# Performance work log

Measured on AMD Instinct MI355X. Metric: run time of the kernel, lower is better.

## Reference

```python
import jax, jax.numpy as jnp
from jax import lax
import numpy as np

B, T, F, H = 64, 512, 256, 512


def _gru_scan(data_tbf, Wi, bi, Wh, bhn):
    """Run a flax-style GRUCell over time. data_tbf: (T, B, F) -> (T, B, H)."""
    def step(h, x):
        xg = x @ Wi + bi              # (B, 3H): ir | iz | in
        hg = h @ Wh                   # (B, 3H): hr | hz | hn (hn bias added below)
        xr, xz, xn = jnp.split(xg, 3, axis=-1)
        hr, hz, hn = jnp.split(hg, 3, axis=-1)
        r = jax.nn.sigmoid(xr + hr)
        z = jax.nn.sigmoid(xz + hz)
        n = jnp.tanh(xn + r * (hn + bhn))
        new_h = (1.0 - z) * n + z * h
        return new_h, new_h

    h0 = jnp.zeros((data_tbf.shape[1], Wh.shape[0]), data_tbf.dtype)
    _, ys = lax.scan(step, h0, data_tbf)
    return ys


def setup_inputs() -> dict:
    key = jax.random.key(0)
    ks = jax.random.split(key, 5)
    s_i = 1.0 / np.sqrt(F)
    s_h = 1.0 / np.sqrt(H)
    return {
        "data": jax.random.normal(ks[0], (B, T, F), jnp.float32),
        "Wi_f": jax.random.normal(ks[1], (F, 3 * H), jnp.float32) * s_i,
        "bi_f": jnp.zeros((3 * H,), jnp.float32),
        "Wh_f": jax.random.normal(ks[2], (H, 3 * H), jnp.float32) * s_h,
        "bhn_f": jnp.zeros((H,), jnp.float32),
        "Wi_b": jax.random.normal(ks[3], (F, 3 * H), jnp.float32) * s_i,
        "bi_b": jnp.zeros((3 * H,), jnp.float32),
        "Wh_b": jax.random.normal(ks[4], (H, 3 * H), jnp.float32) * s_h,
        "bhn_b": jnp.zeros((H,), jnp.float32),
    }


def reference(data, Wi_f, bi_f, Wh_f, bhn_f, Wi_b, bi_b, Wh_b, bhn_b):
    # Forward direction: scan over time (axis 1 of data)
    fwd = _gru_scan(jnp.swapaxes(data, 0, 1), Wi_f, bi_f, Wh_f, bhn_f)
    fwd = jnp.swapaxes(fwd, 0, 1)                      # (B, T, H)
    # 'Backward' direction: source flips axis 0 (batch), faithfully reproduced.
    rev = jnp.flip(data, axis=0)
    bwd = _gru_scan(jnp.swapaxes(rev, 0, 1), Wi_b, bi_b, Wh_b, bhn_b)
    bwd = jnp.swapaxes(bwd, 0, 1)                      # (B, T, H)
    bwd = jnp.flip(bwd, axis=0)
    return jnp.concatenate([fwd, bwd], axis=-1)        # (B, T, 2H)
```

## Files before the change

### kernel.cpp

```cpp
#include <hip/hip_runtime.h>
#include <hip/hip_bf16.h>


#define TT 512
#define FF 256
#define HH 512
#define G3 1536
#define NSLICE 32
#define NWG 256
#define NTHR 64

typedef __attribute__((ext_vector_type(8))) short short8;
typedef __attribute__((ext_vector_type(4))) float f32x4;

__device__ __forceinline__ unsigned short f2bf(float f) {
  union { float f; unsigned u; } x; x.f = f;
  return (unsigned short)((x.u + 0x7fffu + ((x.u >> 16) & 1u)) >> 16);
}

__device__ __forceinline__ unsigned pk2(float a, float b) {
  union { __hip_bfloat162 h; unsigned u; } x;
  x.h = __float22bfloat162_rn(make_float2(a, b));
  return x.u;
}

__device__ __forceinline__ float sigm(float x) {
  return __builtin_amdgcn_rcpf(1.f + __expf(-x));
}

#define MFMA(a, b, c) __builtin_amdgcn_mfma_f32_16x16x32_bf16((a), (b), (c), 0, 0, 0)

__global__ __launch_bounds__(NTHR, 1) void gru_fused(
    const float* __restrict__ data,
    const float* __restrict__ Wi_f, const float* __restrict__ bi_f,
    const float* __restrict__ Wh_f, const float* __restrict__ bhn_f,
    const float* __restrict__ Wi_b, const float* __restrict__ bi_b,
    const float* __restrict__ Wh_b, const float* __restrict__ bhn_b,
    float* __restrict__ out,
    unsigned long long* __restrict__ hbuf,
    int* __restrict__ flags)
{
  const int wg   = blockIdx.x;
  const int unit = wg & 7;
  const int s    = wg >> 3;
  const int dir  = unit >> 2;
  const int bg   = unit & 3;
  const int lane = threadIdx.x;
  const int l15  = lane & 15;
  const int lg   = lane >> 4;

  const float* Wi  = dir ? Wi_b  : Wi_f;
  const float* Wh  = dir ? Wh_b  : Wh_f;
  const float* bi  = dir ? bi_b  : bi_f;
  const float* bhn = dir ? bhn_b : bhn_f;

  const int colT = s * 16 + l15;
  const int colBase = s * 16 + lg * 4;

  short8 whf[3][16];
#pragma unroll
  for (int g = 0; g < 3; ++g)
#pragma unroll
    for (int ks = 0; ks < 16; ++ks) {
      short8 v;
#pragma unroll
      for (int j = 0; j < 8; ++j)
        v[j] = (short)f2bf(Wh[(size_t)(ks * 32 + lg * 8 + j) * G3 + g * HH + colT]);
      whf[g][ks] = v;
    }
  short8 wif[3][8];
#pragma unroll
  for (int g = 0; g < 3; ++g)
#pragma unroll
    for (int ks = 0; ks < 8; ++ks) {
      short8 v;
#pragma unroll
      for (int j = 0; j < 8; ++j)
        v[j] = (short)f2bf(Wi[(size_t)(ks * 32 + lg * 8 + j) * G3 + g * HH + colT]);
      wif[g][ks] = v;
    }
  float biR[4], biZ[4], biN[4], bhc[4];
#pragma unroll
  for (int j = 0; j < 4; ++j) {
    biR[j] = bi[colBase + j];
    biZ[j] = bi[HH + colBase + j];
    biN[j] = bi[2 * HH + colBase + j];
    bhc[j] = bhn[colBase + j];
  }

  int* myflags = flags + unit * 32;
  const float* xbase = data + (size_t)(bg * 16 + l15) * TT * FF;

  float hp[4] = {0.f, 0.f, 0.f, 0.f};

  for (int t = 0; t < TT; ++t) {
    const int ib = t & 1;

    f32x4 accR = {0.f, 0.f, 0.f, 0.f};
    f32x4 accZ = {0.f, 0.f, 0.f, 0.f};
    f32x4 xN   = {0.f, 0.f, 0.f, 0.f};
    {
      const float* xr = xbase + (size_t)t * FF;
#pragma unroll
      for (int ks = 0; ks < 8; ++ks) {
        float4 x0 = *(const float4*)(xr + ks * 32 + lg * 8);
        float4 x1 = *(const float4*)(xr + ks * 32 + lg * 8 + 4);
        union { short8 s; unsigned u[4]; } a;
        a.u[0] = pk2(x0.x, x0.y); a.u[1] = pk2(x0.z, x0.w);
        a.u[2] = pk2(x1.x, x1.y); a.u[3] = pk2(x1.z, x1.w);
        accR = MFMA(wif[0][ks], a.s, accR);
        accZ = MFMA(wif[1][ks], a.s, accZ);
        xN   = MFMA(wif[2][ks], a.s, xN);
      }
    }

    if (t > 0) {
      const int fidx = lane & 31;
      while (true) {
        int fl = __hip_atomic_load(&myflags[fidx], __ATOMIC_RELAXED, __HIP_MEMORY_SCOPE_AGENT);
        if (__all(fl >= t)) break;
      }
      asm volatile("" ::: "memory");
    }

    const unsigned long long* hin = hbuf + (size_t)(unit * 2 + ib) * 2048;
    unsigned long long q[32];
#pragma unroll
    for (int ks = 0; ks < 16; ++ks) {
      const int bidx = l15 * 128 + ks * 8 + lg * 2;
      q[2 * ks]     = __hip_atomic_load(&hin[bidx],     __ATOMIC_RELAXED, __HIP_MEMORY_SCOPE_AGENT);
      q[2 * ks + 1] = __hip_atomic_load(&hin[bidx + 1], __ATOMIC_RELAXED, __HIP_MEMORY_SCOPE_AGENT);
    }

    f32x4 hN = {0.f, 0.f, 0.f, 0.f};
#pragma unroll
    for (int ks = 0; ks < 16; ++ks) {
      union { short8 s; unsigned long long q[2]; } a;
      a.q[0] = q[2 * ks]; a.q[1] = q[2 * ks + 1];
      accR = MFMA(whf[0][ks], a.s, accR);
      accZ = MFMA(whf[1][ks], a.s, accZ);
      hN   = MFMA(whf[2][ks], a.s, hN);
    }

    float hv[4];
#pragma unroll
    for (int j = 0; j < 4; ++j) {
      float r = sigm(accR[j] + biR[j]);
      float z = sigm(accZ[j] + biZ[j]);
      float e = __expf(2.f * (xN[j] + biN[j] + r * (hN[j] + bhc[j])));
      float n = 1.f - 2.f * __builtin_amdgcn_rcpf(e + 1.f);
      hv[j] = (1.f - z) * n + z * hp[j];
      hp[j] = hv[j];
    }

    unsigned long long pv = (unsigned long long)pk2(hv[0], hv[1])
                          | ((unsigned long long)pk2(hv[2], hv[3]) << 32);
    unsigned long long* hout = hbuf + (size_t)(unit * 2 + (ib ^ 1)) * 2048;
    __hip_atomic_store(&hout[l15 * 128 + s * 4 + lg], pv,
                       __ATOMIC_RELAXED, __HIP_MEMORY_SCOPE_AGENT);
    asm volatile("s_waitcnt vmcnt(0)" ::: "memory");
    if (lane == 0)
      __hip_atomic_store(&myflags[s], t + 1, __ATOMIC_RELAXED, __HIP_MEMORY_SCOPE_AGENT);

    *(float4*)(out + ((size_t)(bg * 16 + l15) * TT + t) * 1024 + (size_t)dir * HH + colBase)
        = make_float4(hv[0], hv[1], hv[2], hv[3]);
  }
}

extern "C" void kernel_launch(void* const* d_in, const int* in_sizes, int n_in,
                              void* d_out, int out_size, void* d_ws, size_t ws_size,
                              hipStream_t stream) {
  const float* data  = (const float*)d_in[0];
  const float* Wi_f  = (const float*)d_in[1];
  const float* bi_f  = (const float*)d_in[2];
  const float* Wh_f  = (const float*)d_in[3];
  const float* bhn_f = (const float*)d_in[4];
  const float* Wi_b  = (const float*)d_in[5];
  const float* bi_b  = (const float*)d_in[6];
  const float* Wh_b  = (const float*)d_in[7];
  const float* bhn_b = (const float*)d_in[8];
  float* out = (float*)d_out;

  unsigned long long* hbuf = (unsigned long long*)d_ws;
  int* flags = (int*)((char*)d_ws + 262144);
  hipMemsetAsync(d_ws, 0, 262144 + 4096, stream);

  gru_fused<<<NWG, NTHR, 0, stream>>>(data, Wi_f, bi_f, Wh_f, bhn_f,
                                      Wi_b, bi_b, Wh_b, bhn_b, out, hbuf, flags);
}
```

Before: 3.732 ms.

## Replace flag-based step barrier with per-element tagged hidden-state exchange

Drops the separate per-slice flag array and the store-wait-then-flag handshake. Each bf16 hidden value is now packed with a 16-bit timestep tag in a 32-bit word, and readers poll the hidden buffer itself with cache-bypassing loads until every tag matches. This takes a full memory round trip (vmcnt wait plus flag publish) off the serial critical path of each timestep. In exchange the exchange buffer doubles in size, the polling loads reread the whole hidden vector on each retry, and correctness relies on each 64-bit half being stored atomically with its tags.

```diff
diff --git a/kernel.cpp b/kernel.cpp
--- a/kernel.cpp
+++ b/kernel.cpp
@@ -6,12 +6,15 @@
 #define FF 256
 #define HH 512
 #define G3 1536
-#define NSLICE 32
 #define NWG 256
 #define NTHR 64
 
 typedef __attribute__((ext_vector_type(8))) short short8;
 typedef __attribute__((ext_vector_type(4))) float f32x4;
+typedef unsigned int u32;
+typedef unsigned long long u64;
+
+union U4 { uint4 v; u32 u[4]; u64 q[2]; };
 
 __device__ __forceinline__ unsigned short f2bf(float f) {
   union { float f; unsigned u; } x; x.f = f;
@@ -37,8 +40,7 @@
     const float* __restrict__ Wi_b, const float* __restrict__ bi_b,
     const float* __restrict__ Wh_b, const float* __restrict__ bhn_b,
     float* __restrict__ out,
-    unsigned long long* __restrict__ hbuf,
-    int* __restrict__ flags)
+    u32* __restrict__ hbuf)
 {
   const int wg   = blockIdx.x;
   const int unit = wg & 7;
@@ -88,14 +90,10 @@
     bhc[j] = bhn[colBase + j];
   }
 
-  int* myflags = flags + unit * 32;
   const float* xbase = data + (size_t)(bg * 16 + l15) * TT * FF;
-
   float hp[4] = {0.f, 0.f, 0.f, 0.f};
 
   for (int t = 0; t < TT; ++t) {
-    const int ib = t & 1;
-
     f32x4 accR = {0.f, 0.f, 0.f, 0.f};
     f32x4 accZ = {0.f, 0.f, 0.f, 0.f};
     f32x4 xN   = {0.f, 0.f, 0.f, 0.f};
@@ -114,29 +112,38 @@
       }
     }
 
-    if (t > 0) {
-      const int fidx = lane & 31;
-      while (true) {
-        int fl = __hip_atomic_load(&myflags[fidx], __ATOMIC_RELAXED, __HIP_MEMORY_SCOPE_AGENT);
-        if (__all(fl >= t)) break;
+    const u32 tag = (u32)t;
+    const u32* hb = hbuf + ((size_t)(unit * 2 + (t & 1)) << 13);
+    U4 q[32];
+    while (true) {
+#pragma unroll
+      for (int ks = 0; ks < 16; ++ks) {
+        const u32* p = hb + l15 * 512 + ks * 32 + lg * 8;
+        asm volatile("global_load_dwordx4 %0, %1, off sc0 sc1"
+                     : "=v"(q[2 * ks].v) : "v"(p));
+        asm volatile("global_load_dwordx4 %0, %1, off sc0 sc1"
+                     : "=v"(q[2 * ks + 1].v) : "v"(p + 4));
       }
-      asm volatile("" ::: "memory");
-    }
-
-    const unsigned long long* hin = hbuf + (size_t)(unit * 2 + ib) * 2048;
-    unsigned long long q[32];
+      asm volatile("s_waitcnt vmcnt(0)" ::: "memory");
+      u32 bad = 0;
 #pragma unroll
-    for (int ks = 0; ks < 16; ++ks) {
-      const int bidx = l15 * 128 + ks * 8 + lg * 2;
-      q[2 * ks]     = __hip_atomic_load(&hin[bidx],     __ATOMIC_RELAXED, __HIP_MEMORY_SCOPE_AGENT);
-      q[2 * ks + 1] = __hip_atomic_load(&hin[bidx + 1], __ATOMIC_RELAXED, __HIP_MEMORY_SCOPE_AGENT);
+      for (int c = 0; c < 32; ++c) {
+        bad |= (q[c].u[0] ^ tag) & 0xffffu;
+        bad |= (q[c].u[3] ^ tag) & 0xffffu;
+      }
+      if (__all(bad == 0)) break;
     }
 
     f32x4 hN = {0.f, 0.f, 0.f, 0.f};
 #pragma unroll
     for (int ks = 0; ks < 16; ++ks) {
-      union { short8 s; unsigned long long q[2]; } a;
-      a.q[0] = q[2 * ks]; a.q[1] = q[2 * ks + 1];
+      union { short8 s; unsigned u[4]; } a;
+#pragma unroll
+      for (int i = 0; i < 2; ++i) {
+        const U4& c = q[2 * ks + i];
+        a.u[2 * i]     = __builtin_amdgcn_perm(c.u[1], c.u[0], 0x07060302u);
+        a.u[2 * i + 1] = __builtin_amdgcn_perm(c.u[3], c.u[2], 0x07060302u);
+      }
       accR = MFMA(whf[0][ks], a.s, accR);
       accZ = MFMA(whf[1][ks], a.s, accZ);
       hN   = MFMA(whf[2][ks], a.s, hN);
@@ -153,14 +160,17 @@
       hp[j] = hv[j];
     }
 
-    unsigned long long pv = (unsigned long long)pk2(hv[0], hv[1])
-                          | ((unsigned long long)pk2(hv[2], hv[3]) << 32);
-    unsigned long long* hout = hbuf + (size_t)(unit * 2 + (ib ^ 1)) * 2048;
-    __hip_atomic_store(&hout[l15 * 128 + s * 4 + lg], pv,
-                       __ATOMIC_RELAXED, __HIP_MEMORY_SCOPE_AGENT);
-    asm volatile("s_waitcnt vmcnt(0)" ::: "memory");
-    if (lane == 0)
-      __hip_atomic_store(&myflags[s], t + 1, __ATOMIC_RELAXED, __HIP_MEMORY_SCOPE_AGENT);
+    {
+      U4 w;
+      const u32 wtag = (u32)(t + 1);
+#pragma unroll
+      for (int j = 0; j < 4; ++j)
+        w.u[j] = ((u32)f2bf(hv[j]) << 16) | wtag;
+      u32* ho = hbuf + ((size_t)(unit * 2 + ((t + 1) & 1)) << 13);
+      u64* pdst = (u64*)(ho + l15 * 512 + s * 16 + lg * 4);
+      __hip_atomic_store(&pdst[0], w.q[0], __ATOMIC_RELAXED, __HIP_MEMORY_SCOPE_AGENT);
+      __hip_atomic_store(&pdst[1], w.q[1], __ATOMIC_RELAXED, __HIP_MEMORY_SCOPE_AGENT);
+    }
 
     *(float4*)(out + ((size_t)(bg * 16 + l15) * TT + t) * 1024 + (size_t)dir * HH + colBase)
         = make_float4(hv[0], hv[1], hv[2], hv[3]);
@@ -181,10 +191,9 @@
   const float* bhn_b = (const float*)d_in[8];
   float* out = (float*)d_out;
 
-  unsigned long long* hbuf = (unsigned long long*)d_ws;
-  int* flags = (int*)((char*)d_ws + 262144);
-  hipMemsetAsync(d_ws, 0, 262144 + 4096, stream);
+  u32* hbuf = (u32*)d_ws;
+  (void)hipMemsetAsync(d_ws, 0, 524288, stream);
 
   gru_fused<<<NWG, NTHR, 0, stream>>>(data, Wi_f, bi_f, Wh_f, bhn_f,
-                                      Wi_b, bi_b, Wh_b, bhn_b, out, hbuf, flags);
+                                      Wi_b, bi_b, Wh_b, bhn_b, out, hbuf);
 }
```

Result: no change. 3.747 ms (+0.4%).

## Exchange hidden state through output buffer instead of separate bf16 scratch

Applied to the files above, without the earlier changes.

Removes the double-buffered bf16 hidden-state scratch. Each workgroup now writes its fp32 hidden slice straight into the output tensor, and consumers read the previous timestep's row from the output and convert it to bf16 locally. The flag poll becomes inline asm with sc0 sc1 cache bypass. This drops a redundant store per step and shrinks the memset, but it doubles the bytes read per step (fp32 instead of bf16) and adds conversion work on the recurrent critical path.

```diff
diff --git a/kernel.cpp b/kernel.cpp
--- a/kernel.cpp
+++ b/kernel.cpp
@@ -6,12 +6,13 @@
 #define FF 256
 #define HH 512
 #define G3 1536
-#define NSLICE 32
 #define NWG 256
 #define NTHR 64
 
 typedef __attribute__((ext_vector_type(8))) short short8;
 typedef __attribute__((ext_vector_type(4))) float f32x4;
+typedef unsigned int u32;
+typedef unsigned long long u64;
 
 __device__ __forceinline__ unsigned short f2bf(float f) {
   union { float f; unsigned u; } x; x.f = f;
@@ -37,8 +38,7 @@
     const float* __restrict__ Wi_b, const float* __restrict__ bi_b,
     const float* __restrict__ Wh_b, const float* __restrict__ bhn_b,
     float* __restrict__ out,
-    unsigned long long* __restrict__ hbuf,
-    int* __restrict__ flags)
+    u32* __restrict__ flags)
 {
   const int wg   = blockIdx.x;
   const int unit = wg & 7;
@@ -88,14 +88,14 @@
     bhc[j] = bhn[colBase + j];
   }
 
-  int* myflags = flags + unit * 32;
   const float* xbase = data + (size_t)(bg * 16 + l15) * TT * FF;
+  const float* hbase = out + (size_t)(bg * 16 + l15) * TT * 1024 + (size_t)dir * HH;
+  u32* myflags = flags + unit * 32;
+  const u32* fp = myflags + (lane & 31);
 
   float hp[4] = {0.f, 0.f, 0.f, 0.f};
 
   for (int t = 0; t < TT; ++t) {
-    const int ib = t & 1;
-
     f32x4 accR = {0.f, 0.f, 0.f, 0.f};
     f32x4 accZ = {0.f, 0.f, 0.f, 0.f};
     f32x4 xN   = {0.f, 0.f, 0.f, 0.f};
@@ -114,32 +114,29 @@
       }
     }
 
+    f32x4 hN = {0.f, 0.f, 0.f, 0.f};
     if (t > 0) {
-      const int fidx = lane & 31;
+      u32 fl;
       while (true) {
-        int fl = __hip_atomic_load(&myflags[fidx], __ATOMIC_RELAXED, __HIP_MEMORY_SCOPE_AGENT);
-        if (__all(fl >= t)) break;
+        asm volatile("global_load_dword %0, %1, off sc0 sc1"
+                     : "=v"(fl) : "v"(fp));
+        asm volatile("s_waitcnt vmcnt(0)" ::: "memory");
+        if (__all(fl >= (u32)t)) break;
       }
       asm volatile("" ::: "memory");
-    }
 
-    const unsigned long long* hin = hbuf + (size_t)(unit * 2 + ib) * 2048;
-    unsigned long long q[32];
+      const float* hr = hbase + (size_t)(t - 1) * 1024;
 #pragma unroll
-    for (int ks = 0; ks < 16; ++ks) {
-      const int bidx = l15 * 128 + ks * 8 + lg * 2;
-      q[2 * ks]     = __hip_atomic_load(&hin[bidx],     __ATOMIC_RELAXED, __HIP_MEMORY_SCOPE_AGENT);
-      q[2 * ks + 1] = __hip_atomic_load(&hin[bidx + 1], __ATOMIC_RELAXED, __HIP_MEMORY_SCOPE_AGENT);
-    }
-
-    f32x4 hN = {0.f, 0.f, 0.f, 0.f};
-#pragma unroll
-    for (int ks = 0; ks < 16; ++ks) {
-      union { short8 s; unsigned long long q[2]; } a;
-      a.q[0] = q[2 * ks]; a.q[1] = q[2 * ks + 1];
-      accR = MFMA(whf[0][ks], a.s, accR);
-      accZ = MFMA(whf[1][ks], a.s, accZ);
-      hN   = MFMA(whf[2][ks], a.s, hN);
+      for (int ks = 0; ks < 16; ++ks) {
+        float4 h0 = *(const float4*)(hr + ks * 32 + lg * 8);
+        float4 h1 = *(const float4*)(hr + ks * 32 + lg * 8 + 4);
+        union { short8 s; unsigned u[4]; } a;
+        a.u[0] = pk2(h0.x, h0.y); a.u[1] = pk2(h0.z, h0.w);
+        a.u[2] = pk2(h1.x, h1.y); a.u[3] = pk2(h1.z, h1.w);
+        accR = MFMA(whf[0][ks], a.s, accR);
+        accZ = MFMA(whf[1][ks], a.s, accZ);
+        hN   = MFMA(whf[2][ks], a.s, hN);
+      }
     }
 
     float hv[4];
@@ -153,17 +150,19 @@
       hp[j] = hv[j];
     }
 
-    unsigned long long pv = (unsigned long long)pk2(hv[0], hv[1])
-                          | ((unsigned long long)pk2(hv[2], hv[3]) << 32);
-    unsigned long long* hout = hbuf + (size_t)(unit * 2 + (ib ^ 1)) * 2048;
-    __hip_atomic_store(&hout[l15 * 128 + s * 4 + lg], pv,
-                       __ATOMIC_RELAXED, __HIP_MEMORY_SCOPE_AGENT);
-    asm volatile("s_waitcnt vmcnt(0)" ::: "memory");
-    if (lane == 0)
-      __hip_atomic_store(&myflags[s], t + 1, __ATOMIC_RELAXED, __HIP_MEMORY_SCOPE_AGENT);
-
-    *(float4*)(out + ((size_t)(bg * 16 + l15) * TT + t) * 1024 + (size_t)dir * HH + colBase)
-        = make_float4(hv[0], hv[1], hv[2], hv[3]);
+    {
+      union { float f[2]; u64 q; } p0, p1;
+      p0.f[0] = hv[0]; p0.f[1] = hv[1];
+      p1.f[0] = hv[2]; p1.f[1] = hv[3];
+      u64* po = (u64*)(out + ((size_t)(bg * 16 + l15) * TT + t) * 1024
+                       + (size_t)dir * HH + colBase);
+      __hip_atomic_store(&po[0], p0.q, __ATOMIC_RELAXED, __HIP_MEMORY_SCOPE_AGENT);
+      __hip_atomic_store(&po[1], p1.q, __ATOMIC_RELAXED, __HIP_MEMORY_SCOPE_AGENT);
+      asm volatile("s_waitcnt vmcnt(0)" ::: "memory");
+      if (lane == 0)
+        __hip_atomic_store(&myflags[s], (u32)(t + 1),
+                           __ATOMIC_RELAXED, __HIP_MEMORY_SCOPE_AGENT);
+    }
   }
 }
 
@@ -181,10 +180,9 @@
   const float* bhn_b = (const float*)d_in[8];
   float* out = (float*)d_out;
 
-  unsigned long long* hbuf = (unsigned long long*)d_ws;
-  int* flags = (int*)((char*)d_ws + 262144);
-  hipMemsetAsync(d_ws, 0, 262144 + 4096, stream);
+  u32* flags = (u32*)d_ws;
+  (void)hipMemsetAsync(d_ws, 0, 1024, stream);
 
   gru_fused<<<NWG, NTHR, 0, stream>>>(data, Wi_f, bi_f, Wh_f, bhn_f,
-                                      Wi_b, bi_b, Wh_b, bhn_b, out, hbuf, flags);
+                                      Wi_b, bi_b, Wh_b, bhn_b, out, flags);
 }
```

Measured after the change: 5.363 ms. 43.7% more time.
